# Kernel optimization log

Measured on AMD Instinct MI355X. Metric: run time of the kernel, lower is better.

Reference implementation:

```python
import jax, jax.numpy as jnp
import numpy as np

D_IN, D_DICT, K, N = 768, 16384, 32, 8192


def setup_inputs() -> dict:
    key = jax.random.key(0)
    k1, k2, k3, k4, k5 = jax.random.split(key, 5)
    s_in = 1.0 / np.sqrt(D_IN)
    s_dict = 1.0 / np.sqrt(D_DICT)
    return {
        "x": jax.random.normal(k1, (N, D_IN), dtype=jnp.float32),
        # torch Linear: weight [out, in], bias [out]
        "W_enc": jax.random.uniform(k2, (D_DICT, D_IN), jnp.float32, -s_in, s_in),
        "b_enc": jax.random.uniform(k3, (D_DICT,), jnp.float32, -s_in, s_in),
        "W_dec": jax.random.uniform(k4, (D_IN, D_DICT), jnp.float32, -s_dict, s_dict),
        "b_dec": jax.random.uniform(k5, (D_IN,), jnp.float32, -s_dict, s_dict),
    }


def reference(x, W_enc, b_enc, W_dec, b_dec):
    # encode: z = x @ W_enc^T + b_enc  -> [N, d_dict]
    z = jnp.einsum("nd,kd->nk", x, W_enc) + b_enc
    # top-k mask along last dim (scatter 1.0 at top-k indices)
    _, idx = jax.lax.top_k(z, K)                      # idx: [N, K]
    rows = jnp.arange(z.shape[0])[:, None]            # [N, 1]
    mask = jnp.zeros_like(z).at[rows, idx].set(1.0)
    z_sparse = z * mask
    # decode: x_hat = z_sparse @ W_dec^T + b_dec -> [N, d_in]
    x_hat = jnp.einsum("nk,dk->nd", z_sparse, W_dec) + b_dec
    return (x_hat, z_sparse)
```

## Files before the change

kernel.cpp:

```cpp
#include <hip/hip_runtime.h>
#include <stdint.h>

#define D_IN   768
#define D_DICT 16384
#define NROWS  8192
#define TOPK   32
#define CAND_TARGET 40
#define CAND_MAX    80
#define FLOORU 0xBF60u
#define NTILES 128
#define SEG    32
#define LECAP  3072

typedef __attribute__((ext_vector_type(4))) float  f32x4;
typedef __attribute__((ext_vector_type(8))) short  s16x8;
typedef __attribute__((ext_vector_type(4))) unsigned short u16x4;

static __device__ __forceinline__ unsigned short f2bf(float f) {
    unsigned int u = __float_as_uint(f);
    unsigned int r = (u + 0x7FFFu + ((u >> 16) & 1u)) >> 16;
    return (unsigned short)r;
}
static __device__ __forceinline__ unsigned short bfmap(unsigned short u) {
    return (u & 0x8000u) ? (unsigned short)(~u) : (unsigned short)(u | 0x8000u);
}

static __device__ __forceinline__ void gload_lds16(const void* g, void* l) {
    __builtin_amdgcn_global_load_lds(
        (const __attribute__((address_space(1))) unsigned int*)g,
        (__attribute__((address_space(3))) unsigned int*)l, 16, 0, 0);
}

__global__ __launch_bounds__(256) void cast_bf16(const float4* __restrict__ in,
                                                 u16x4* __restrict__ out, int n4) {
    int idx = blockIdx.x * 256 + threadIdx.x;
    if (idx >= n4) return;
    float4 v = in[idx];
    u16x4 o;
    o.x = f2bf(v.x); o.y = f2bf(v.y); o.z = f2bf(v.z); o.w = f2bf(v.w);
    out[idx] = o;
}

__global__ void transpose_wdec(const float* __restrict__ in, float* __restrict__ out) {
    __shared__ float t[32][33];
    int bx = blockIdx.x, by = blockIdx.y;
    int tx = threadIdx.x, ty = threadIdx.y;
#pragma unroll
    for (int i = 0; i < 4; ++i)
        t[ty + i * 8][tx] = in[(size_t)(by * 32 + ty + i * 8) * D_DICT + bx * 32 + tx];
    __syncthreads();
#pragma unroll
    for (int i = 0; i < 4; ++i)
        out[(size_t)(bx * 32 + ty + i * 8) * D_IN + by * 32 + tx] = t[tx][ty + i * 8];
}

__global__ __launch_bounds__(256) void gemm_enc(const unsigned short* __restrict__ Xb,
                                                const unsigned short* __restrict__ Wb,
                                                const float* __restrict__ bEnc,
                                                unsigned int* __restrict__ list,
                                                unsigned char* __restrict__ cnt8,
                                                float* __restrict__ zsp) {
    __shared__ unsigned short As[128 * 64];
    __shared__ unsigned short Bs[128 * 64];
    const int tid    = threadIdx.x;
    const int waveId = tid >> 6;
    const int lane   = tid & 63;
    const int rowBase = blockIdx.y * 128;
    const int colBase = blockIdx.x * 128;
    const int wm = waveId >> 1, wn = waveId & 1;

    {
        float4 z4 = make_float4(0.f, 0.f, 0.f, 0.f);
        float4* zd = (float4*)(zsp + (size_t)rowBase * D_DICT + colBase);
#pragma unroll
        for (int i = 0; i < 16; ++i) {
            int slot = i * 256 + tid;
            int rr = slot >> 5;
            int cc = slot & 31;
            zd[(size_t)rr * (D_DICT / 4) + cc] = z4;
        }
    }

    f32x4 acc[4][4] = {};

    const int m0 = wm * 64 + (lane & 15);
    const int n0 = wn * 64 + (lane & 15);
    const int quad = lane >> 4;
    const int xa = m0 & 7;
    const int xb = n0 & 7;

    for (int k0 = 0; k0 < D_IN; k0 += 64) {
#pragma unroll
        for (int i = 0; i < 4; ++i) {
            int slot = i * 256 + tid;
            int r = slot >> 3;
            int cc = ((slot & 7) ^ (r & 7)) * 8;
            const unsigned short* ga = Xb + (size_t)(rowBase + r) * D_IN + k0 + cc;
            const unsigned short* gb = Wb + (size_t)(colBase + r) * D_IN + k0 + cc;
            unsigned short* la = As + (size_t)(i * 256 + waveId * 64) * 8;
            unsigned short* lb = Bs + (size_t)(i * 256 + waveId * 64) * 8;
            gload_lds16(ga, la);
            gload_lds16(gb, lb);
        }
        __syncthreads();
#pragma unroll
        for (int kk = 0; kk < 2; ++kk) {
            const int ch = kk * 4 + quad;
            s16x8 a[4], b[4];
#pragma unroll
            for (int t = 0; t < 4; ++t) {
                a[t] = *(const s16x8*)(As + (m0 + t * 16) * 64 + ((ch ^ xa) << 3));
                b[t] = *(const s16x8*)(Bs + (n0 + t * 16) * 64 + ((ch ^ xb) << 3));
            }
#pragma unroll
            for (int mi = 0; mi < 4; ++mi)
#pragma unroll
                for (int ni = 0; ni < 4; ++ni)
                    acc[mi][ni] = __builtin_amdgcn_mfma_f32_16x16x32_bf16(
                        a[mi], b[ni], acc[mi][ni], 0, 0, 0);
        }
        __syncthreads();
    }

    int*          lcnt  = (int*)Bs;
    unsigned int* stage = (unsigned int*)As;
    if (tid < 128) lcnt[tid] = 0;
    __syncthreads();

    const int col0 = colBase + wn * 64 + (lane & 15);
    const int rq   = (lane >> 4) * 4;
    float bias[4];
#pragma unroll
    for (int ni = 0; ni < 4; ++ni) bias[ni] = bEnc[col0 + ni * 16];
#pragma unroll
    for (int mi = 0; mi < 4; ++mi) {
#pragma unroll
        for (int rg = 0; rg < 4; ++rg) {
            const int lrow = wm * 64 + mi * 16 + rq + rg;
            unsigned int uv[4];
            unsigned int m4 = 0;
#pragma unroll
            for (int ni = 0; ni < 4; ++ni) {
                float v = acc[mi][ni][rg] + bias[ni];
                unsigned int u = bfmap(f2bf(v));
                uv[ni] = (u << 16) | (unsigned int)(col0 + ni * 16);
                m4 |= (u >= FLOORU) ? (1u << ni) : 0u;
            }
            if (m4) {
                int c = __popc(m4);
                int pos = atomicAdd(&lcnt[lrow], c);
#pragma unroll
                for (int ni = 0; ni < 4; ++ni) {
                    if (m4 & (1u << ni)) {
                        int off = __popc(m4 & ((1u << ni) - 1u));
                        if (pos + off < SEG) stage[lrow * SEG + pos + off] = uv[ni];
                    }
                }
            }
        }
    }
    __syncthreads();

    const int colTile = blockIdx.x;
    if (tid < 128) {
        int c = lcnt[tid]; if (c > SEG) c = SEG;
        cnt8[(size_t)(rowBase + tid) * NTILES + colTile] = (unsigned char)c;
    }
#pragma unroll
    for (int i = 0; i < 16; ++i) {
        int slot = i * 256 + tid;
        int r = slot >> 5, s = slot & 31;
        int c = lcnt[r]; if (c > SEG) c = SEG;
        if (s < c)
            list[((size_t)(rowBase + r) * NTILES + colTile) * SEG + s] = stage[r * SEG + s];
    }
}

__global__ __launch_bounds__(256) void sel_dec(const unsigned int* __restrict__ list,
                                               const unsigned char* __restrict__ cnt8,
                                               const float* __restrict__ x,
                                               const float* __restrict__ wEnc,
                                               const float* __restrict__ bEnc,
                                               const float* __restrict__ wDecT,
                                               const float* __restrict__ bDec,
                                               float* __restrict__ zsp,
                                               float* __restrict__ xhat) {
    const int row = blockIdx.x;
    const int tid = threadIdx.x;
    const int waveId = tid >> 6;

    __shared__ int   histc[4][256];
    alignas(16) __shared__ float xs[D_IN];
    __shared__ unsigned int le[LECAP];
    __shared__ unsigned int cw[NTILES / 4];
    __shared__ int   tb[NTILES];
    __shared__ int   cidx[CAND_MAX];
    __shared__ float zc[CAND_MAX];
    __shared__ int   selk[TOPK];
    __shared__ float selv[TOPK];
    __shared__ int   sh_ncand, sh_bin, sh_cum, sh_bin2;
    __shared__ int   sh_nstrict, sh_ntie, sh_nsel;

    if (tid < NTILES / 4)
        cw[tid] = ((const unsigned int*)(cnt8 + (size_t)row * NTILES))[tid];
    if (tid < 192)
        ((float4*)xs)[tid] = ((const float4*)(x + (size_t)row * D_IN))[tid];
    if (tid == 0) { sh_nstrict = 0; sh_ntie = 0; sh_nsel = 0; sh_bin = -1; }
    __syncthreads();

    const unsigned char* cb = (const unsigned char*)cw;
    if (tid < 64) {
        int c0 = cb[2 * tid], c1 = cb[2 * tid + 1];
        int s = c0 + c1;
        int pref = s;
#pragma unroll
        for (int off = 1; off < 64; off <<= 1) {
            int n = __shfl_up(pref, off, 64);
            if (tid >= off) pref += n;
        }
        int base0 = pref - s;
        tb[2 * tid] = base0;
        tb[2 * tid + 1] = base0 + c0;
        if (tid == 63) sh_ncand = pref;
    }
    for (int b = tid; b < 1024; b += 256) ((int*)histc)[b] = 0;
    __syncthreads();
    const int nCand = min(sh_ncand, LECAP);

    for (int i = tid; i < NTILES * SEG; i += 256) {
        int t = i >> 5, s = i & 31;
        if (s < (int)cb[t]) {
            int dst = tb[t] + s;
            if (dst < LECAP) le[dst] = list[((size_t)row * NTILES + t) * SEG + s];
        }
    }
    __syncthreads();

    const int T = CAND_TARGET;
    for (int i = tid; i < nCand; i += 256) {
        unsigned int u = le[i] >> 16;
        int bin = (int)((u - FLOORU) >> 6);
        if (bin > 255) bin = 255;
        atomicAdd(&histc[waveId][bin], 1);
    }
    __syncthreads();
    if (tid < 256) histc[0][tid] += histc[1][tid] + histc[2][tid] + histc[3][tid];
    __syncthreads();
    if (tid < 64) {
        int l = tid;
        int b0 = 255 - l * 4;
        int s0 = histc[0][b0], s1 = histc[0][b0 - 1],
            s2 = histc[0][b0 - 2], s3 = histc[0][b0 - 3];
        int local = s0 + s1 + s2 + s3;
        int pref = local;
#pragma unroll
        for (int off = 1; off < 64; off <<= 1) {
            int n = __shfl_up(pref, off, 64);
            if (l >= off) pref += n;
        }
        unsigned long long m = __ballot(pref >= T);
        if (m) {
            int first = (int)__ffsll(m) - 1;
            if (l == first) {
                int cum = pref - local;
                int b, c;
                if      (cum + s0 >= T)           { b = b0;     c = cum; }
                else if (cum + s0 + s1 >= T)      { b = b0 - 1; c = cum + s0; }
                else if (cum + s0 + s1 + s2 >= T) { b = b0 - 2; c = cum + s0 + s1; }
                else                              { b = b0 - 3; c = cum + s0 + s1 + s2; }
                sh_bin = b; sh_cum = c;
            }
        }
    }
    __syncthreads();
    const int b1 = sh_bin;
    unsigned int tieLo, tieTop;

    if (b1 >= 0) {
        const int cumAbove = sh_cum;
        for (int b = tid; b < 1024; b += 256) ((int*)histc)[b] = 0;
        __syncthreads();
        for (int i = tid; i < nCand; i += 256) {
            unsigned int u = le[i] >> 16;
            int bin = (int)((u - FLOORU) >> 6);
            if (bin > 255) bin = 255;
            if (bin == b1) atomicAdd(&histc[waveId][(u - FLOORU) & 63u], 1);
        }
        __syncthreads();
        if (tid < 64) {
            int l = tid;
            int bb = 63 - l;
            int local = histc[0][bb] + histc[1][bb] + histc[2][bb] + histc[3][bb];
            int pref = local;
#pragma unroll
            for (int off = 1; off < 64; off <<= 1) {
                int n = __shfl_up(pref, off, 64);
                if (l >= off) pref += n;
            }
            unsigned long long m = __ballot(cumAbove + pref >= T);
            int first = (int)__ffsll(m) - 1;
            if (l == first) sh_bin2 = bb;
        }
        __syncthreads();
        tieLo  = FLOORU + ((unsigned)b1 << 6) + (unsigned)sh_bin2;
        tieTop = tieLo;
    } else {
        tieLo = 1u; tieTop = 0u;
    }

    for (int i = tid; i < nCand; i += 256) {
        unsigned int u = le[i] >> 16;
        int col = (int)(le[i] & 0xFFFFu);
        if (u > tieTop) {
            int p = atomicAdd(&sh_nstrict, 1);
            cidx[p] = col;
        } else if (u >= tieLo) {
            int t = atomicAdd(&sh_ntie, 1);
            if (t < CAND_TARGET) cidx[CAND_MAX - 1 - t] = col;
        }
    }
    __syncthreads();
    const int nstrict = sh_nstrict;
    const int nt = min(sh_ntie, CAND_TARGET);
    int tmpv = 0;
    if (tid < nt) tmpv = cidx[CAND_MAX - 1 - tid];
    __syncthreads();
    if (tid < nt) cidx[nstrict + tid] = tmpv;
    __syncthreads();
    const int nc = nstrict + nt;

    const int sub = tid & 7;
    const int cq  = tid >> 3;
    for (int c0 = 0; c0 < nc; c0 += 32) {
        int c = c0 + cq;
        double a0 = 0.0, a1 = 0.0, a2 = 0.0, a3 = 0.0;
        int k = 0;
        if (c < nc) {
            k = cidx[c];
            const float4* wp = (const float4*)(wEnc + (size_t)k * D_IN);
            const float4* xp = (const float4*)xs;
#pragma unroll 8
            for (int j = 0; j < 24; ++j) {
                float4 wv = wp[j * 8 + sub];
                float4 xv = xp[j * 8 + sub];
                a0 += (double)xv.x * (double)wv.x;
                a1 += (double)xv.y * (double)wv.y;
                a2 += (double)xv.z * (double)wv.z;
                a3 += (double)xv.w * (double)wv.w;
            }
        }
        double acc = (a0 + a1) + (a2 + a3);
        acc += __shfl_xor(acc, 1, 64);
        acc += __shfl_xor(acc, 2, 64);
        acc += __shfl_xor(acc, 4, 64);
        if (c < nc && sub == 0) zc[c] = (float)(acc + (double)bEnc[k]);
    }
    __syncthreads();

    if (tid < nc) {
        float v = zc[tid];
        int   k = cidx[tid];
        int rk = 0;
        for (int j = 0; j < nc; ++j) {
            float vj = zc[j];
            if (vj > v || (vj == v && cidx[j] < k)) ++rk;
        }
        if (rk < TOPK) {
            int s = atomicAdd(&sh_nsel, 1);
            selk[s] = k; selv[s] = v;
        }
    }
    __syncthreads();

    if (tid < TOPK) zsp[(size_t)row * D_DICT + selk[tid]] = selv[tid];

    if (tid < 192) {
        float4 acc = ((const float4*)bDec)[tid];
#pragma unroll 8
        for (int j = 0; j < TOPK; ++j) {
            const float4* wr = (const float4*)(wDecT + (size_t)selk[j] * D_IN);
            float4 wv = wr[tid];
            float s = selv[j];
            acc.x += s * wv.x; acc.y += s * wv.y;
            acc.z += s * wv.z; acc.w += s * wv.w;
        }
        ((float4*)(xhat + (size_t)row * D_IN))[tid] = acc;
    }
}

extern "C" void kernel_launch(void* const* d_in, const int* in_sizes, int n_in,
                              void* d_out, int out_size, void* d_ws, size_t ws_size,
                              hipStream_t stream) {
    const float* x    = (const float*)d_in[0];
    const float* wEnc = (const float*)d_in[1];
    const float* bEnc = (const float*)d_in[2];
    const float* wDec = (const float*)d_in[3];
    const float* bDec = (const float*)d_in[4];

    float* xhat = (float*)d_out;
    float* zsp  = (float*)d_out + (size_t)NROWS * D_IN;

    char* ws = (char*)d_ws;
    unsigned short* Xb   = (unsigned short*)ws;
    unsigned short* Wb   = (unsigned short*)(ws + (size_t)NROWS * D_IN * 2);
    float*          WdT  = (float*)(ws + (size_t)NROWS * D_IN * 2
                                       + (size_t)D_DICT * D_IN * 2);
    unsigned int*   list = (unsigned int*)(ws + 88080384);
    unsigned char*  cnt8 = (unsigned char*)(ws + 88080384
                                       + (size_t)NROWS * NTILES * SEG * 4);

    {
        int n4 = NROWS * D_IN / 4;
        cast_bf16<<<(n4 + 255) / 256, 256, 0, stream>>>((const float4*)x, (u16x4*)Xb, n4);
    }
    {
        int n4 = D_DICT * D_IN / 4;
        cast_bf16<<<(n4 + 255) / 256, 256, 0, stream>>>((const float4*)wEnc, (u16x4*)Wb, n4);
    }
    transpose_wdec<<<dim3(D_DICT / 32, D_IN / 32), dim3(32, 8), 0, stream>>>(wDec, WdT);
    gemm_enc<<<dim3(D_DICT / 128, NROWS / 128), 256, 0, stream>>>(Xb, Wb, bEnc, list, cnt8, zsp);
    sel_dec<<<NROWS, 256, 0, stream>>>(list, cnt8, x, wEnc, bEnc, WdT, bDec, zsp, xhat);
}
```

Baseline: 1.393 ms.

## Enlarge encoder GEMM tiles to 256x256 with double-buffered LDS and wave-ballot compaction

The encoder GEMM moves from 128x128 tiles with 4 waves to 256x256 tiles with 8 waves, each wave computing 128x64. LDS staging is now double-buffered so the next K-slice loads while MFMAs run, and blocks are remapped across XCDs through a swizzled linear grid. Candidate compaction replaces per-lane atomics with ballot-based prefix counts and one atomic per row group. Column tiles drop to 64 with 48-slot segments, and sel_dec is adjusted to match. The larger tiles raise register and LDS pressure (128KB dynamic LDS), which risks lower occupancy and overflow of the per-tile candidate segments.

```diff
diff --git a/kernel.cpp b/kernel.cpp
--- a/kernel.cpp
+++ b/kernel.cpp
@@ -8,9 +8,14 @@
 #define CAND_TARGET 40
 #define CAND_MAX    80
 #define FLOORU 0xBF60u
-#define NTILES 128
-#define SEG    32
+#define NTILES 64
+#define SEG    48
 #define LECAP  3072
+
+#define BM 256
+#define BN 256
+#define BK 64
+#define NKT (D_IN / BK)
 
 typedef __attribute__((ext_vector_type(4))) float  f32x4;
 typedef __attribute__((ext_vector_type(8))) short  s16x8;
@@ -54,66 +59,80 @@
         out[(size_t)(bx * 32 + ty + i * 8) * D_IN + by * 32 + tx] = t[tx][ty + i * 8];
 }
 
-__global__ __launch_bounds__(256) void gemm_enc(const unsigned short* __restrict__ Xb,
-                                                const unsigned short* __restrict__ Wb,
-                                                const float* __restrict__ bEnc,
-                                                unsigned int* __restrict__ list,
-                                                unsigned char* __restrict__ cnt8,
-                                                float* __restrict__ zsp) {
-    __shared__ unsigned short As[128 * 64];
-    __shared__ unsigned short Bs[128 * 64];
+__global__ __launch_bounds__(512, 2) void gemm_enc(const unsigned short* __restrict__ Xb,
+                                                   const unsigned short* __restrict__ Wb,
+                                                   const float* __restrict__ bEnc,
+                                                   unsigned int* __restrict__ list,
+                                                   unsigned char* __restrict__ cnt8,
+                                                   float* __restrict__ zsp) {
+    extern __shared__ char smem[];
+    unsigned short* As = (unsigned short*)smem;
+    unsigned short* Bs = (unsigned short*)(smem + 2 * BM * BK * 2);
     const int tid    = threadIdx.x;
     const int waveId = tid >> 6;
     const int lane   = tid & 63;
-    const int rowBase = blockIdx.y * 128;
-    const int colBase = blockIdx.x * 128;
-    const int wm = waveId >> 1, wn = waveId & 1;
+
+    const int wg    = blockIdx.x;
+    const int wgid  = (wg & 7) * 256 + (wg >> 3);
+    const int ctile = wgid & (NTILES - 1);
+    const int rtile = wgid >> 6;
+    const int rowBase = rtile * BM;
+    const int colBase = ctile * BN;
+    const int wm = waveId >> 2, wn = waveId & 3;
 
     {
         float4 z4 = make_float4(0.f, 0.f, 0.f, 0.f);
         float4* zd = (float4*)(zsp + (size_t)rowBase * D_DICT + colBase);
 #pragma unroll
-        for (int i = 0; i < 16; ++i) {
-            int slot = i * 256 + tid;
-            int rr = slot >> 5;
-            int cc = slot & 31;
-            zd[(size_t)rr * (D_DICT / 4) + cc] = z4;
-        }
-    }
-
-    f32x4 acc[4][4] = {};
-
-    const int m0 = wm * 64 + (lane & 15);
-    const int n0 = wn * 64 + (lane & 15);
+        for (int i = 0; i < 32; ++i) {
+            int slot = i * 512 + tid;
+            zd[(size_t)(slot >> 6) * (D_DICT / 4) + (slot & 63)] = z4;
+        }
+    }
+
+    f32x4 acc[8][4] = {};
+
+    const int m0 = wm * 128 + (lane & 15);
+    const int n0 = wn * 64  + (lane & 15);
     const int quad = lane >> 4;
-    const int xa = m0 & 7;
-    const int xb = n0 & 7;
-
-    for (int k0 = 0; k0 < D_IN; k0 += 64) {
+    const int xsw  = lane & 7;
+
+    auto STAGE = [&](int p, int t) {
+        const int k0 = t * BK;
+        unsigned short* Ab = As + (size_t)p * (BM * BK);
+        unsigned short* Bb = Bs + (size_t)p * (BN * BK);
 #pragma unroll
         for (int i = 0; i < 4; ++i) {
-            int slot = i * 256 + tid;
-            int r = slot >> 3;
-            int cc = ((slot & 7) ^ (r & 7)) * 8;
-            const unsigned short* ga = Xb + (size_t)(rowBase + r) * D_IN + k0 + cc;
-            const unsigned short* gb = Wb + (size_t)(colBase + r) * D_IN + k0 + cc;
-            unsigned short* la = As + (size_t)(i * 256 + waveId * 64) * 8;
-            unsigned short* lb = Bs + (size_t)(i * 256 + waveId * 64) * 8;
-            gload_lds16(ga, la);
-            gload_lds16(gb, lb);
-        }
-        __syncthreads();
+            int slot = i * 512 + tid;
+            int r  = slot >> 3;
+            int lc = (slot & 7) ^ (r & 7);
+            gload_lds16(Xb + (size_t)(rowBase + r) * D_IN + k0 + lc * 8,
+                        Ab + (size_t)(i * 512 + waveId * 64) * 8);
+            gload_lds16(Wb + (size_t)(colBase + r) * D_IN + k0 + lc * 8,
+                        Bb + (size_t)(i * 512 + waveId * 64) * 8);
+        }
+    };
+
+    STAGE(0, 0);
+    __syncthreads();
+
+    for (int t = 0; t < NKT; ++t) {
+        const int p = t & 1;
+        if (t + 1 < NKT) STAGE(p ^ 1, t + 1);
+        const unsigned short* Ab = As + (size_t)p * (BM * BK);
+        const unsigned short* Bb = Bs + (size_t)p * (BN * BK);
 #pragma unroll
         for (int kk = 0; kk < 2; ++kk) {
             const int ch = kk * 4 + quad;
-            s16x8 a[4], b[4];
-#pragma unroll
-            for (int t = 0; t < 4; ++t) {
-                a[t] = *(const s16x8*)(As + (m0 + t * 16) * 64 + ((ch ^ xa) << 3));
-                b[t] = *(const s16x8*)(Bs + (n0 + t * 16) * 64 + ((ch ^ xb) << 3));
-            }
-#pragma unroll
-            for (int mi = 0; mi < 4; ++mi)
+            s16x8 a[8], b[4];
+#pragma unroll
+            for (int f = 0; f < 8; ++f)
+                a[f] = *(const s16x8*)(Ab + (m0 + f * 16) * BK + ((ch ^ xsw) << 3));
+#pragma unroll
+            for (int f = 0; f < 4; ++f)
+                b[f] = *(const s16x8*)(Bb + (n0 + f * 16) * BK + ((ch ^ xsw) << 3));
+#pragma unroll
+            for (int mi = 0; mi < 8; ++mi)
 #pragma unroll
                 for (int ni = 0; ni < 4; ++ni)
                     acc[mi][ni] = __builtin_amdgcn_mfma_f32_16x16x32_bf16(
@@ -122,57 +141,64 @@
         __syncthreads();
     }
 
-    int*          lcnt  = (int*)Bs;
-    unsigned int* stage = (unsigned int*)As;
-    if (tid < 128) lcnt[tid] = 0;
-    __syncthreads();
-
-    const int col0 = colBase + wn * 64 + (lane & 15);
-    const int rq   = (lane >> 4) * 4;
+    int*          lcnt  = (int*)smem;
+    unsigned int* stage = (unsigned int*)(smem + 1024);
+    if (tid < 256) lcnt[tid] = 0;
+    __syncthreads();
+
+    const int colW = colBase + wn * 64 + (lane & 15);
     float bias[4];
 #pragma unroll
-    for (int ni = 0; ni < 4; ++ni) bias[ni] = bEnc[col0 + ni * 16];
-#pragma unroll
-    for (int mi = 0; mi < 4; ++mi) {
+    for (int f = 0; f < 4; ++f) bias[f] = bEnc[colW + f * 16];
+    const unsigned long long qmask = 0xFFFFull << (quad * 16);
+    const unsigned long long lmask = (1ull << lane) - 1ull;
+
+#pragma unroll
+    for (int mi = 0; mi < 8; ++mi) {
 #pragma unroll
         for (int rg = 0; rg < 4; ++rg) {
-            const int lrow = wm * 64 + mi * 16 + rq + rg;
+            const int lrow = wm * 128 + mi * 16 + quad * 4 + rg;
             unsigned int uv[4];
-            unsigned int m4 = 0;
-#pragma unroll
-            for (int ni = 0; ni < 4; ++ni) {
-                float v = acc[mi][ni][rg] + bias[ni];
+            unsigned long long bm[4];
+            int m4 = 0;
+#pragma unroll
+            for (int f = 0; f < 4; ++f) {
+                float v = acc[mi][f][rg] + bias[f];
                 unsigned int u = bfmap(f2bf(v));
-                uv[ni] = (u << 16) | (unsigned int)(col0 + ni * 16);
-                m4 |= (u >= FLOORU) ? (1u << ni) : 0u;
+                uv[f] = (u << 16) | (unsigned int)(colW + f * 16);
+                bool pass = (u >= FLOORU);
+                bm[f] = __ballot(pass);
+                if (pass) m4 |= (1 << f);
             }
+            int rowTotal = (int)(__popcll(bm[0] & qmask) + __popcll(bm[1] & qmask)
+                               + __popcll(bm[2] & qmask) + __popcll(bm[3] & qmask));
+            int base = 0;
+            if ((lane & 15) == 0 && rowTotal) base = atomicAdd(&lcnt[lrow], rowTotal);
+            base = __shfl(base, quad * 16, 64);
             if (m4) {
-                int c = __popc(m4);
-                int pos = atomicAdd(&lcnt[lrow], c);
-#pragma unroll
-                for (int ni = 0; ni < 4; ++ni) {
-                    if (m4 & (1u << ni)) {
-                        int off = __popc(m4 & ((1u << ni) - 1u));
-                        if (pos + off < SEG) stage[lrow * SEG + pos + off] = uv[ni];
+                int pre = 0;
+#pragma unroll
+                for (int f = 0; f < 4; ++f) {
+                    if (m4 & (1 << f)) {
+                        int pos = base + pre + (int)__popcll(bm[f] & qmask & lmask);
+                        if (pos < SEG) stage[lrow * SEG + pos] = uv[f];
                     }
+                    pre += (int)__popcll(bm[f] & qmask);
                 }
             }
         }
     }
     __syncthreads();
 
-    const int colTile = blockIdx.x;
-    if (tid < 128) {
+    if (tid < 256) {
         int c = lcnt[tid]; if (c > SEG) c = SEG;
-        cnt8[(size_t)(rowBase + tid) * NTILES + colTile] = (unsigned char)c;
-    }
-#pragma unroll
-    for (int i = 0; i < 16; ++i) {
-        int slot = i * 256 + tid;
-        int r = slot >> 5, s = slot & 31;
+        cnt8[(size_t)(rowBase + tid) * NTILES + ctile] = (unsigned char)c;
+    }
+    for (int i = tid; i < 256 * SEG; i += 512) {
+        int r = i / SEG, s = i - r * SEG;
         int c = lcnt[r]; if (c > SEG) c = SEG;
         if (s < c)
-            list[((size_t)(rowBase + r) * NTILES + colTile) * SEG + s] = stage[r * SEG + s];
+            list[((size_t)(rowBase + r) * NTILES + ctile) * SEG + s] = stage[r * SEG + s];
     }
 }
 
@@ -210,17 +236,14 @@
 
     const unsigned char* cb = (const unsigned char*)cw;
     if (tid < 64) {
-        int c0 = cb[2 * tid], c1 = cb[2 * tid + 1];
-        int s = c0 + c1;
-        int pref = s;
+        int c = cb[tid];
+        int pref = c;
 #pragma unroll
         for (int off = 1; off < 64; off <<= 1) {
             int n = __shfl_up(pref, off, 64);
             if (tid >= off) pref += n;
         }
-        int base0 = pref - s;
-        tb[2 * tid] = base0;
-        tb[2 * tid + 1] = base0 + c0;
+        tb[tid] = pref - c;
         if (tid == 63) sh_ncand = pref;
     }
     for (int b = tid; b < 1024; b += 256) ((int*)histc)[b] = 0;
@@ -228,7 +251,7 @@
     const int nCand = min(sh_ncand, LECAP);
 
     for (int i = tid; i < NTILES * SEG; i += 256) {
-        int t = i >> 5, s = i & 31;
+        int t = i / SEG, s = i - t * SEG;
         if (s < (int)cb[t]) {
             int dst = tb[t] + s;
             if (dst < LECAP) le[dst] = list[((size_t)row * NTILES + t) * SEG + s];
@@ -409,6 +432,13 @@
     unsigned char*  cnt8 = (unsigned char*)(ws + 88080384
                                        + (size_t)NROWS * NTILES * SEG * 4);
 
+    static int configured = 0;
+    if (!configured) {
+        hipFuncSetAttribute((const void*)gemm_enc,
+                            hipFuncAttributeMaxDynamicSharedMemorySize, 131072);
+        configured = 1;
+    }
+
     {
         int n4 = NROWS * D_IN / 4;
         cast_bf16<<<(n4 + 255) / 256, 256, 0, stream>>>((const float4*)x, (u16x4*)Xb, n4);
@@ -418,6 +448,6 @@
         cast_bf16<<<(n4 + 255) / 256, 256, 0, stream>>>((const float4*)wEnc, (u16x4*)Wb, n4);
     }
     transpose_wdec<<<dim3(D_DICT / 32, D_IN / 32), dim3(32, 8), 0, stream>>>(wDec, WdT);
-    gemm_enc<<<dim3(D_DICT / 128, NROWS / 128), 256, 0, stream>>>(Xb, Wb, bEnc, list, cnt8, zsp);
+    gemm_enc<<<(NROWS / BM) * (D_DICT / BN), 512, 131072, stream>>>(Xb, Wb, bEnc, list, cnt8, zsp);
     sel_dec<<<NROWS, 256, 0, stream>>>(list, cnt8, x, wEnc, bEnc, WdT, bDec, zsp, xhat);
 }
```

Result: faster. 1.309 ms (-6.0%).
